# Performance work log

Hardware: AMD Instinct MI355X
Metric: run time of the kernel (lower is better)

## Reference

```python
import jax, jax.numpy as jnp
import numpy as np

B, T, C = 4, 1024, 1024
H, HKV, N = 16, 8, 64
REP = H // HKV
D_LORA, D_MV, D_GATE = 64, 32, 160
EPS = 1e-06
ROPE_THETA = 1000000.0


def setup_inputs() -> dict:
    key = jax.random.key(0)
    ks = jax.random.split(key, 20)
    def s(i, shape, sc=0.02, off=0.0):
        return jax.random.normal(ks[i], shape, jnp.float32) * sc + off
    return {
        "x": jax.random.normal(ks[0], (B, T, C), jnp.float32),
        "v_first": jax.random.normal(ks[1], (B, T, C), jnp.float32),
        "Wr": s(2, (C, H * N)), "Wk": s(3, (C, HKV * N)), "Wv": s(4, (C, HKV * N)), "Wo": s(5, (H * N, C)),
        "w0": s(6, (C,), 0.1, -4.0), "w1": s(7, (C, D_LORA)), "w2": s(8, (D_LORA, C)),
        "a0": s(9, (C,), 0.1), "a1": s(10, (C, D_LORA)), "a2": s(11, (D_LORA, C)),
        "v0": s(12, (C,), 0.1, 0.73), "v1": s(13, (C, D_MV)), "v2": s(14, (D_MV, C)),
        "g1": s(15, (C, D_GATE)), "g2": s(16, (D_GATE, C)),
        "r_k": s(17, (H, N), 0.1, -0.04),
        "r_norm_w": jnp.ones((N,), jnp.float32), "k_norm_w": jnp.ones((N,), jnp.float32),
    }


def rms_norm(x, w):
    var = jnp.mean(jnp.square(x.astype(jnp.float32)), axis=-1, keepdims=True)
    return w * (x.astype(jnp.float32) * jax.lax.rsqrt(var + EPS))


def rope_cos_sin(t, n):
    half = n // 2
    inv_freq = 1.0 / ROPE_THETA ** (jnp.arange(half, dtype=jnp.float32) / half)
    freqs = jnp.arange(t, dtype=jnp.float32)[:, None] * inv_freq[None, :]
    emb = jnp.concatenate([freqs, freqs], axis=-1)  # [T, N]
    # broadcast to [1, T, 1, N] (unsqueeze_dim=2 in the original)
    return jnp.cos(emb)[None, :, None, :], jnp.sin(emb)[None, :, None, :]


def rotate_half(x):
    x1, x2 = jnp.split(x, 2, axis=-1)
    return jnp.concatenate([-x2, x1], axis=-1)


def wkv7(r, dec, k, v, a, b):
    # RWKV-7 state recurrence. All inputs [B,T,H,N]; state S: [B,H,N_v,N_k].
    # S_t = S_{t-1} * diag(dec_t) + (S_{t-1} @ a_t) b_t^T + v_t k_t^T ; y_t = S_t r_t
    def step(S, ins):
        rt, wt, kt, vt, at, bt = ins  # each [B,H,N]
        S = S * wt[:, :, None, :] \
            + jnp.einsum('bhij,bhj,bhk->bhik', S, at, bt) \
            + vt[..., None] * kt[..., None, :]
        return S, jnp.einsum('bhij,bhj->bhi', S, rt)
    ins = tuple(jnp.moveaxis(t, 1, 0) for t in (r, dec, k, v, a, b))  # [T,B,H,N]
    S0 = jnp.zeros((r.shape[0], H, N, N), r.dtype)
    _, ys = jax.lax.scan(step, S0, ins)
    return jnp.moveaxis(ys, 0, 1)  # [B,T,H,N]


def _forward(x, v_first, Wr, Wk, Wv, Wo, w0, w1, w2, a0, a1, a2, v0, v1, v2, g1, g2, r_k, r_norm_w, k_norm_w):
    Bq, Tq = x.shape[0], x.shape[1]
    r = rms_norm((x @ Wr).reshape(Bq, Tq, H, N), r_norm_w)
    k = rms_norm((x @ Wk).reshape(Bq, Tq, HKV, N), k_norm_w)
    # w = -softplus(-(w0 + tanh(x@w1)@w2)) - 0.5 ; kernel decay = exp(-exp(w))
    w = -jax.nn.softplus(-(w0 + jnp.tanh(x @ w1) @ w2)) - 0.5  # [B,T,C]
    v = (x @ Wv).reshape(Bq, Tq, HKV, N)
    cos, sin = rope_cos_sin(Tq, N)
    r = r * cos + rotate_half(r) * sin
    k = k * cos + rotate_half(k) * sin
    k = jnp.repeat(k, REP, axis=2)  # GQA repeat -> [B,T,H,N]
    v = jnp.repeat(v, REP, axis=2)
    # layer_id != 0: residual value mixing with first-layer value
    mix = jax.nn.sigmoid(v0 + (x @ v1) @ v2).reshape(Bq, Tq, H, N)
    v = v + (v_first.reshape(Bq, Tq, H, N) - v) * mix
    a = jax.nn.sigmoid(a0 + (x @ a1) @ a2).reshape(Bq, Tq, H, N)
    g = jax.nn.sigmoid(x @ g1) @ g2  # [B,T,C]
    kk = k / jnp.maximum(jnp.linalg.norm(k, axis=-1, keepdims=True), 1e-12)  # F.normalize per head
    dec = jnp.exp(-jnp.exp(w)).reshape(Bq, Tq, H, N)
    y = wkv7(r, dec, k, v, -kk, kk * a)  # [B,T,H,N]
    y = y + jnp.sum(r * k * r_k, axis=-1, keepdims=True) * v
    out = (y.reshape(Bq, Tq, H * N) * g) @ Wo
    return out


def reference(x, v_first, Wr, Wk, Wv, Wo, w0, w1, w2, a0, a1, a2, v0, v1, v2, g1, g2, r_k, r_norm_w, k_norm_w):
    out = _forward(x, v_first, Wr, Wk, Wv, Wo, w0, w1, w2, a0, a1, a2, v0, v1, v2, g1, g2, r_k, r_norm_w, k_norm_w)
    return (out, v_first)
```

## Files before the change

### kernel.cpp

```cpp
#include <hip/hip_runtime.h>
#include <math.h>
#include <stdint.h>

#define Bb   4
#define Tt   1024
#define Cc   1024
#define Hh   16
#define HKVn 8
#define Nn   64
#define MT   (Bb*Tt)
#define NC   32
#define CL   32
#define NCAT 2432

typedef __bf16 bf16x8_t __attribute__((ext_vector_type(8)));
typedef float  f32x4_t  __attribute__((ext_vector_type(4)));

__device__ __forceinline__ uint16_t f2bf(float f) {
    uint32_t u = __float_as_uint(f);
    uint32_t r = (u + 0x7fffu + ((u >> 16) & 1u)) >> 16;
    return (uint16_t)r;
}

__device__ __forceinline__ float rlane(float v, int l) {
    return __uint_as_float(__builtin_amdgcn_readlane(__float_as_uint(v), l));
}

__device__ __forceinline__ void stage64(const float* g, float* l, int lane) {
    __builtin_amdgcn_global_load_lds(
        (const __attribute__((address_space(1))) uint32_t*)(g + lane),
        (__attribute__((address_space(3))) uint32_t*)l, 4, 0, 0);
}

__global__ __launch_bounds__(256) void conv_copy_kernel(
    const float* __restrict__ x, uint16_t* __restrict__ xb,
    const float4* __restrict__ vfi, float4* __restrict__ out2, int n4)
{
    int i = blockIdx.x * blockDim.x + threadIdx.x;
    if (i >= n4) return;
    float4 v = reinterpret_cast<const float4*>(x)[i];
    ushort4 o;
    o.x = f2bf(v.x); o.y = f2bf(v.y); o.z = f2bf(v.z); o.w = f2bf(v.w);
    reinterpret_cast<ushort4*>(xb)[i] = o;
    out2[i] = vfi[i];
}

__global__ __launch_bounds__(256) void transpose_all_kernel(
    const float* __restrict__ Wr, const float* __restrict__ Wk, const float* __restrict__ Wv,
    const float* __restrict__ w1, const float* __restrict__ a1, const float* __restrict__ v1,
    const float* __restrict__ g1, const float* __restrict__ Wo,
    const float* __restrict__ w2, const float* __restrict__ a2,
    const float* __restrict__ v2, const float* __restrict__ g2,
    uint16_t* __restrict__ WCAT, uint16_t* __restrict__ WoT,
    uint16_t* __restrict__ LW, uint16_t* __restrict__ LA,
    uint16_t* __restrict__ LV, uint16_t* __restrict__ LG)
{
    int z = blockIdx.z;
    const float* W; int Nsrc, Ndst, Ksrc, Kout, off; uint16_t* out;
    switch (z) {
        case 0:  W = Wr; Nsrc = 1024; Ndst = 1024; Ksrc = 1024; Kout = 1024; off = 0;    out = WCAT; break;
        case 1:  W = Wk; Nsrc = 512;  Ndst = 512;  Ksrc = 1024; Kout = 1024; off = 1024; out = WCAT; break;
        case 2:  W = Wv; Nsrc = 512;  Ndst = 512;  Ksrc = 1024; Kout = 1024; off = 1536; out = WCAT; break;
        case 3:  W = w1; Nsrc = 64;   Ndst = 64;   Ksrc = 1024; Kout = 1024; off = 2048; out = WCAT; break;
        case 4:  W = a1; Nsrc = 64;   Ndst = 64;   Ksrc = 1024; Kout = 1024; off = 2112; out = WCAT; break;
        case 5:  W = v1; Nsrc = 32;   Ndst = 64;   Ksrc = 1024; Kout = 1024; off = 2176; out = WCAT; break;
        case 6:  W = g1; Nsrc = 160;  Ndst = 192;  Ksrc = 1024; Kout = 1024; off = 2240; out = WCAT; break;
        case 7:  W = Wo; Nsrc = 1024; Ndst = 1024; Ksrc = 1024; Kout = 1024; off = 0;    out = WoT;  break;
        case 8:  W = w2; Nsrc = 1024; Ndst = 1024; Ksrc = 64;   Kout = 64;   off = 0;    out = LW;   break;
        case 9:  W = a2; Nsrc = 1024; Ndst = 1024; Ksrc = 64;   Kout = 64;   off = 0;    out = LA;   break;
        case 10: W = v2; Nsrc = 1024; Ndst = 1024; Ksrc = 32;   Kout = 64;   off = 0;    out = LV;   break;
        default: W = g2; Nsrc = 1024; Ndst = 1024; Ksrc = 160;  Kout = 192;  off = 0;    out = LG;   break;
    }
    int n0 = blockIdx.x * 32, k0 = blockIdx.y * 32;
    if (n0 >= Ndst || k0 >= Kout) return;
    __shared__ float tile[32][33];
    int tx = threadIdx.x & 31, ty = threadIdx.x >> 5;
    #pragma unroll
    for (int i = 0; i < 32; i += 8) {
        int k = k0 + ty + i, n = n0 + tx;
        tile[ty + i][tx] = (k < Ksrc && n < Nsrc) ? W[(size_t)k * Nsrc + n] : 0.f;
    }
    __syncthreads();
    #pragma unroll
    for (int i = 0; i < 32; i += 8) {
        int n = n0 + ty + i, k = k0 + tx;
        if (n < Ndst) out[(size_t)(off + n) * Kout + k] = f2bf(tile[tx][ty + i]);
    }
}

__global__ __launch_bounds__(256) void gemm_bf16_proj(
    const uint16_t* __restrict__ A, const uint16_t* __restrict__ Bt,
    int M, int N, int K,
    float* __restrict__ R_, float* __restrict__ K_, float* __restrict__ V_,
    uint16_t* __restrict__ W1b, uint16_t* __restrict__ A1b,
    uint16_t* __restrict__ V1b, uint16_t* __restrict__ G1b)
{
    __shared__ __align__(16) uint16_t As[128 * 64];
    __shared__ __align__(16) uint16_t Bs[128 * 64];
    int tid  = threadIdx.x;
    int lane = tid & 63, wid = tid >> 6;
    int wm = (wid >> 1) * 64, wn = (wid & 1) * 64;
    int bm = blockIdx.y * 128, bn = blockIdx.x * 128;

    f32x4_t acc[4][4];
    #pragma unroll
    for (int i = 0; i < 4; ++i)
        #pragma unroll
        for (int j = 0; j < 4; ++j)
            #pragma unroll
            for (int e = 0; e < 4; ++e) acc[i][j][e] = 0.f;

    int rowS[4], kbS[4];
    #pragma unroll
    for (int i = 0; i < 4; ++i) {
        int d = (i * 256 + tid) * 16;
        int row = d >> 7;
        int kb = (d & 127) ^ ((row & 7) << 4);
        rowS[i] = row; kbS[i] = kb >> 1;
    }

    for (int k0 = 0; k0 < K; k0 += 64) {
        #pragma unroll
        for (int i = 0; i < 4; ++i) {
            const uint16_t* srcA = A + (size_t)(bm + rowS[i]) * K + k0 + kbS[i];
            uint16_t* ldsA = As + (i * 256 + wid * 64) * 8;
            __builtin_amdgcn_global_load_lds(
                (const __attribute__((address_space(1))) uint32_t*)srcA,
                (__attribute__((address_space(3))) uint32_t*)ldsA, 16, 0, 0);
            int nr = bn + rowS[i];
            const uint16_t* srcB = Bt + (size_t)(nr < N ? nr : 0) * K + k0 + kbS[i];
            uint16_t* ldsB = Bs + (i * 256 + wid * 64) * 8;
            __builtin_amdgcn_global_load_lds(
                (const __attribute__((address_space(1))) uint32_t*)srcB,
                (__attribute__((address_space(3))) uint32_t*)ldsB, 16, 0, 0);
        }
        __syncthreads();

        #pragma unroll
        for (int kk = 0; kk < 64; kk += 32) {
            int fb = (kk + ((lane >> 4) << 3)) << 1;
            bf16x8_t af[4], bfr[4];
            #pragma unroll
            for (int i = 0; i < 4; ++i) {
                int row = wm + i * 16 + (lane & 15);
                int byteA = (row << 7) + (fb ^ ((row & 7) << 4));
                af[i] = *reinterpret_cast<const bf16x8_t*>(
                    reinterpret_cast<const char*>(As) + byteA);
                int col = wn + i * 16 + (lane & 15);
                int byteB = (col << 7) + (fb ^ ((col & 7) << 4));
                bfr[i] = *reinterpret_cast<const bf16x8_t*>(
                    reinterpret_cast<const char*>(Bs) + byteB);
            }
            #pragma unroll
            for (int i = 0; i < 4; ++i)
                #pragma unroll
                for (int j = 0; j < 4; ++j)
                    acc[i][j] = __builtin_amdgcn_mfma_f32_16x16x32_bf16(
                        af[i], bfr[j], acc[i][j], 0, 0, 0);
        }
        __syncthreads();
    }

    #pragma unroll
    for (int i = 0; i < 4; ++i) {
        int row0 = bm + wm + i * 16 + ((lane >> 4) << 2);
        #pragma unroll
        for (int j = 0; j < 4; ++j) {
            int col = bn + wn + j * 16 + (lane & 15);
            if (col >= N) continue;
            #pragma unroll
            for (int rg = 0; rg < 4; ++rg) {
                float v = acc[i][j][rg];
                int row = row0 + rg;
                if (col < 1024)       R_[(size_t)row * 1024 + col] = v;
                else if (col < 1536)  K_[(size_t)row * 512 + (col - 1024)] = v;
                else if (col < 2048)  V_[(size_t)row * 512 + (col - 1536)] = v;
                else if (col < 2112)  W1b[(size_t)row * 64 + (col - 2048)] = f2bf(tanhf(v));
                else if (col < 2176)  A1b[(size_t)row * 64 + (col - 2112)] = f2bf(v);
                else if (col < 2240)  V1b[(size_t)row * 64 + (col - 2176)] = f2bf(v);
                else                  G1b[(size_t)row * 192 + (col - 2240)] = f2bf(1.f / (1.f + expf(-v)));
            }
        }
    }
}

__global__ __launch_bounds__(256) void gemm_bf16(
    const uint16_t* __restrict__ A, const uint16_t* __restrict__ Bt,
    float* __restrict__ C, int M, int N, int K)
{
    __shared__ __align__(16) uint16_t As[128 * 64];
    __shared__ __align__(16) uint16_t Bs[128 * 64];
    int tid  = threadIdx.x;
    int lane = tid & 63, wid = tid >> 6;
    int wm = (wid >> 1) * 64, wn = (wid & 1) * 64;
    int bm = blockIdx.y * 128, bn = blockIdx.x * 128;

    f32x4_t acc[4][4];
    #pragma unroll
    for (int i = 0; i < 4; ++i)
        #pragma unroll
        for (int j = 0; j < 4; ++j)
            #pragma unroll
            for (int e = 0; e < 4; ++e) acc[i][j][e] = 0.f;

    int rowS[4], kbS[4];
    #pragma unroll
    for (int i = 0; i < 4; ++i) {
        int d = (i * 256 + tid) * 16;
        int row = d >> 7;
        int kb = (d & 127) ^ ((row & 7) << 4);
        rowS[i] = row; kbS[i] = kb >> 1;
    }

    for (int k0 = 0; k0 < K; k0 += 64) {
        #pragma unroll
        for (int i = 0; i < 4; ++i) {
            const uint16_t* srcA = A + (size_t)(bm + rowS[i]) * K + k0 + kbS[i];
            uint16_t* ldsA = As + (i * 256 + wid * 64) * 8;
            __builtin_amdgcn_global_load_lds(
                (const __attribute__((address_space(1))) uint32_t*)srcA,
                (__attribute__((address_space(3))) uint32_t*)ldsA, 16, 0, 0);
            int nr = bn + rowS[i];
            const uint16_t* srcB = Bt + (size_t)(nr < N ? nr : 0) * K + k0 + kbS[i];
            uint16_t* ldsB = Bs + (i * 256 + wid * 64) * 8;
            __builtin_amdgcn_global_load_lds(
                (const __attribute__((address_space(1))) uint32_t*)srcB,
                (__attribute__((address_space(3))) uint32_t*)ldsB, 16, 0, 0);
        }
        __syncthreads();

        #pragma unroll
        for (int kk = 0; kk < 64; kk += 32) {
            int fb = (kk + ((lane >> 4) << 3)) << 1;
            bf16x8_t af[4], bfr[4];
            #pragma unroll
            for (int i = 0; i < 4; ++i) {
                int row = wm + i * 16 + (lane & 15);
                int byteA = (row << 7) + (fb ^ ((row & 7) << 4));
                af[i] = *reinterpret_cast<const bf16x8_t*>(
                    reinterpret_cast<const char*>(As) + byteA);
                int col = wn + i * 16 + (lane & 15);
                int byteB = (col << 7) + (fb ^ ((col & 7) << 4));
                bfr[i] = *reinterpret_cast<const bf16x8_t*>(
                    reinterpret_cast<const char*>(Bs) + byteB);
            }
            #pragma unroll
            for (int i = 0; i < 4; ++i)
                #pragma unroll
                for (int j = 0; j < 4; ++j)
                    acc[i][j] = __builtin_amdgcn_mfma_f32_16x16x32_bf16(
                        af[i], bfr[j], acc[i][j], 0, 0, 0);
        }
        __syncthreads();
    }

    #pragma unroll
    for (int i = 0; i < 4; ++i) {
        int row0 = bm + wm + i * 16 + ((lane >> 4) << 2);
        #pragma unroll
        for (int j = 0; j < 4; ++j) {
            int col = bn + wn + j * 16 + (lane & 15);
            if (col >= N) continue;
            #pragma unroll
            for (int rg = 0; rg < 4; ++rg)
                C[(size_t)(row0 + rg) * N + col] = acc[i][j][rg];
        }
    }
}

__global__ __launch_bounds__(256) void lora2_mfma(
    const uint16_t* __restrict__ W1b, const uint16_t* __restrict__ A1b,
    const uint16_t* __restrict__ V1b, const uint16_t* __restrict__ G1b,
    const uint16_t* __restrict__ LW, const uint16_t* __restrict__ LA,
    const uint16_t* __restrict__ LV, const uint16_t* __restrict__ LG,
    const float* __restrict__ w0, const float* __restrict__ a0, const float* __restrict__ v0,
    const float* __restrict__ VRAW, const float* __restrict__ vfi,
    const float* __restrict__ ABUF,
    float* __restrict__ DEC, float* __restrict__ AARR,
    float* __restrict__ VFIN, float* __restrict__ GARR)
{
    int seg = blockIdx.x & 3;
    int bn = (blockIdx.x >> 2) * 128;
    int bm = blockIdx.y * 128;

    const uint16_t* A; const uint16_t* Bt; int K;
    if (seg == 0)      { A = W1b; Bt = LW; K = 64; }
    else if (seg == 1) { A = A1b; Bt = LA; K = 64; }
    else if (seg == 2) { A = V1b; Bt = LV; K = 64; }
    else               { A = G1b; Bt = LG; K = 192; }

    __shared__ __align__(16) uint16_t As[128 * 64];
    __shared__ __align__(16) uint16_t Bs[128 * 64];
    int tid  = threadIdx.x;
    int lane = tid & 63, wid = tid >> 6;
    int wm = (wid >> 1) * 64, wn = (wid & 1) * 64;

    f32x4_t acc[4][4];
    #pragma unroll
    for (int i = 0; i < 4; ++i)
        #pragma unroll
        for (int j = 0; j < 4; ++j)
            #pragma unroll
            for (int e = 0; e < 4; ++e) acc[i][j][e] = 0.f;

    int rowS[4], kbS[4];
    #pragma unroll
    for (int i = 0; i < 4; ++i) {
        int d = (i * 256 + tid) * 16;
        int row = d >> 7;
        int kb = (d & 127) ^ ((row & 7) << 4);
        rowS[i] = row; kbS[i] = kb >> 1;
    }

    for (int k0 = 0; k0 < K; k0 += 64) {
        #pragma unroll
        for (int i = 0; i < 4; ++i) {
            const uint16_t* srcA = A + (size_t)(bm + rowS[i]) * K + k0 + kbS[i];
            uint16_t* ldsA = As + (i * 256 + wid * 64) * 8;
            __builtin_amdgcn_global_load_lds(
                (const __attribute__((address_space(1))) uint32_t*)srcA,
                (__attribute__((address_space(3))) uint32_t*)ldsA, 16, 0, 0);
            const uint16_t* srcB = Bt + (size_t)(bn + rowS[i]) * K + k0 + kbS[i];
            uint16_t* ldsB = Bs + (i * 256 + wid * 64) * 8;
            __builtin_amdgcn_global_load_lds(
                (const __attribute__((address_space(1))) uint32_t*)srcB,
                (__attribute__((address_space(3))) uint32_t*)ldsB, 16, 0, 0);
        }
        __syncthreads();

        #pragma unroll
        for (int kk = 0; kk < 64; kk += 32) {
            int fb = (kk + ((lane >> 4) << 3)) << 1;
            bf16x8_t af[4], bfr[4];
            #pragma unroll
            for (int i = 0; i < 4; ++i) {
                int row = wm + i * 16 + (lane & 15);
                int byteA = (row << 7) + (fb ^ ((row & 7) << 4));
                af[i] = *reinterpret_cast<const bf16x8_t*>(
                    reinterpret_cast<const char*>(As) + byteA);
                int col = wn + i * 16 + (lane & 15);
                int byteB = (col << 7) + (fb ^ ((col & 7) << 4));
                bfr[i] = *reinterpret_cast<const bf16x8_t*>(
                    reinterpret_cast<const char*>(Bs) + byteB);
            }
            #pragma unroll
            for (int i = 0; i < 4; ++i)
                #pragma unroll
                for (int j = 0; j < 4; ++j)
                    acc[i][j] = __builtin_amdgcn_mfma_f32_16x16x32_bf16(
                        af[i], bfr[j], acc[i][j], 0, 0, 0);
        }
        __syncthreads();
    }

    #pragma unroll
    for (int i = 0; i < 4; ++i) {
        int row0 = bm + wm + i * 16 + ((lane >> 4) << 2);
        #pragma unroll
        for (int j = 0; j < 4; ++j) {
            int col = bn + wn + j * 16 + (lane & 15);
            #pragma unroll
            for (int rg = 0; rg < 4; ++rg) {
                float v = acc[i][j][rg];
                int row = row0 + rg;
                if (seg == 0) {
                    float z = v + w0[col];
                    float sig = 1.f / (1.f + expf(-z));
                    DEC[(size_t)row * 1024 + col] = expf(-0.6065306597f * sig);
                } else if (seg == 1) {
                    float kk = -ABUF[(size_t)row * 512 + ((col >> 7) << 6) + (col & 63)];
                    AARR[(size_t)row * 1024 + col] = kk / (1.f + expf(-(v + a0[col])));
                } else if (seg == 2) {
                    float m = 1.f / (1.f + expf(-(v + v0[col])));
                    float vr = VRAW[(size_t)row * 512 + ((col >> 7) << 6) + (col & 63)];
                    float vf = vfi[(size_t)row * 1024 + col];
                    VFIN[(size_t)row * 1024 + col] = vr + (vf - vr) * m;
                } else {
                    GARR[(size_t)row * 1024 + col] = v;
                }
            }
        }
    }
}

__global__ __launch_bounds__(64) void normrope_prep(
    float* __restrict__ RRAW, float* __restrict__ KRAW,
    float* __restrict__ ABUF,
    const float* __restrict__ rnw, const float* __restrict__ knw,
    const float* __restrict__ rk,
    float* __restrict__ BON)
{
    int blk = blockIdx.x;
    int hk = blk & 7;
    int bt = blk >> 3;
    int b = bt >> 10, t = bt & 1023;
    int lane = threadIdx.x;
    int fi = lane & 31;
    float invf = powf(1.0e6f, -(float)fi * (1.0f / 32.0f));
    float fr = (float)t * invf;
    float c = cosf(fr), s = sinf(fr);

    size_t kidx = ((size_t)bt * 8 + hk) * 64 + lane;
    float k = KRAW[kidx];
    float ss = k * k;
    #pragma unroll
    for (int m = 1; m < 64; m <<= 1) ss += __shfl_xor(ss, m, 64);
    float kn = k * rsqrtf(ss * (1.f / 64.f) + 1e-6f) * knw[lane];
    float kp = __shfl_xor(kn, 32, 64);
    float kroped = fmaf(kn, c, ((lane < 32) ? -kp : kp) * s);
    KRAW[kidx] = kroped;

    float ss2 = kroped * kroped;
    #pragma unroll
    for (int m = 1; m < 64; m <<= 1) ss2 += __shfl_xor(ss2, m, 64);
    float kk = kroped / fmaxf(sqrtf(ss2), 1e-12f);
    ABUF[kidx] = -kk;

    #pragma unroll
    for (int rep = 0; rep < 2; ++rep) {
        int h = hk * 2 + rep;
        size_t cidx = (size_t)bt * 1024 + h * 64 + lane;
        float r = RRAW[cidx];
        float ssr = r * r;
        #pragma unroll
        for (int m = 1; m < 64; m <<= 1) ssr += __shfl_xor(ssr, m, 64);
        float rn = r * rsqrtf(ssr * (1.f / 64.f) + 1e-6f) * rnw[lane];
        float rp = __shfl_xor(rn, 32, 64);
        float rroped = fmaf(rn, c, ((lane < 32) ? -rp : rp) * s);
        RRAW[cidx] = rroped;

        float bon = rroped * kroped * rk[h * 64 + lane];
        #pragma unroll
        for (int m = 1; m < 64; m <<= 1) bon += __shfl_xor(bon, m, 64);
        if (lane == 0) BON[((size_t)(b * 16 + h)) * 1024 + t] = bon;
    }
}

__global__ __launch_bounds__(64) void wkv_pass1(
    const float* __restrict__ R, const float* __restrict__ Kv,
    const float* __restrict__ Ab, const float* __restrict__ Bhat,
    const float* __restrict__ Dd, const float* __restrict__ Vv,
    float* __restrict__ Q, float* __restrict__ Y0,
    float* __restrict__ PLT, float* __restrict__ ZL)
{
    int blk = blockIdx.x;
    int c   = blk & (NC - 1);
    int bh  = blk >> 5;
    int h   = bh & 15;
    int b   = bh >> 4;
    int hk  = h >> 1;
    int lane = threadIdx.x;
    int t0 = c * CL;

    size_t cb = ((size_t)(b * 1024 + t0)) * 1024 + h * 64;
    size_t kb = ((size_t)(b * 1024 + t0)) * 512 + hk * 64;
    size_t qb = (((size_t)bh) * 1024 + t0) * 64;

    __shared__ __align__(16) float sA[2][64], sB[2][64], sD[2][64],
                                   sR[2][64], sK[2][64], sV[2][64];

    float SP[64], SZ[64];
    #pragma unroll
    for (int j = 0; j < 64; ++j) { SP[j] = (j == lane) ? 1.f : 0.f; SZ[j] = 0.f; }

    auto stage = [&](int u, int buf) {
        stage64(Ab   + kb + (size_t)u * 512,  &sA[buf][0], lane);
        stage64(Bhat + cb + (size_t)u * 1024, &sB[buf][0], lane);
        stage64(Dd   + cb + (size_t)u * 1024, &sD[buf][0], lane);
        stage64(R    + cb + (size_t)u * 1024, &sR[buf][0], lane);
        stage64(Kv   + kb + (size_t)u * 512,  &sK[buf][0], lane);
        stage64(Vv   + cb + (size_t)u * 1024, &sV[buf][0], lane);
    };
    stage(0, 0);

    for (int u = 0; u < CL; ++u) {
        int un = (u + 1 < CL) ? u + 1 : u;
        stage(un, (u + 1) & 1);
        asm volatile("s_waitcnt vmcnt(6)" ::: "memory");
        int cur = u & 1;
        float v = sV[cur][lane];

        float pa0 = 0.f, pa1 = 0.f, za0 = 0.f, za1 = 0.f;
        #pragma unroll
        for (int jc = 0; jc < 16; ++jc) {
            float4 a4 = *reinterpret_cast<const float4*>(&sA[cur][jc * 4]);
            pa0 = fmaf(SP[jc*4+0], a4.x, pa0); za0 = fmaf(SZ[jc*4+0], a4.x, za0);
            pa1 = fmaf(SP[jc*4+1], a4.y, pa1); za1 = fmaf(SZ[jc*4+1], a4.y, za1);
            pa0 = fmaf(SP[jc*4+2], a4.z, pa0); za0 = fmaf(SZ[jc*4+2], a4.z, za0);
            pa1 = fmaf(SP[jc*4+3], a4.w, pa1); za1 = fmaf(SZ[jc*4+3], a4.w, za1);
        }
        float pa = pa0 + pa1;
        float za = za0 + za1;

        float q0 = 0.f, q1 = 0.f, y0a = 0.f, y1a = 0.f;
        #pragma unroll
        for (int jc = 0; jc < 16; ++jc) {
            float4 d4 = *reinterpret_cast<const float4*>(&sD[cur][jc * 4]);
            float4 b4 = *reinterpret_cast<const float4*>(&sB[cur][jc * 4]);
            float4 k4 = *reinterpret_cast<const float4*>(&sK[cur][jc * 4]);
            float4 r4 = *reinterpret_cast<const float4*>(&sR[cur][jc * 4]);
            SP[jc*4+0] = fmaf(SP[jc*4+0], d4.x, pa * b4.x); q0  = fmaf(SP[jc*4+0], r4.x, q0);
            SZ[jc*4+0] = fmaf(SZ[jc*4+0], d4.x, fmaf(za, b4.x, v * k4.x)); y0a = fmaf(SZ[jc*4+0], r4.x, y0a);
            SP[jc*4+1] = fmaf(SP[jc*4+1], d4.y, pa * b4.y); q1  = fmaf(SP[jc*4+1], r4.y, q1);
            SZ[jc*4+1] = fmaf(SZ[jc*4+1], d4.y, fmaf(za, b4.y, v * k4.y)); y1a = fmaf(SZ[jc*4+1], r4.y, y1a);
            SP[jc*4+2] = fmaf(SP[jc*4+2], d4.z, pa * b4.z); q0  = fmaf(SP[jc*4+2], r4.z, q0);
            SZ[jc*4+2] = fmaf(SZ[jc*4+2], d4.z, fmaf(za, b4.z, v * k4.z)); y0a = fmaf(SZ[jc*4+2], r4.z, y0a);
            SP[jc*4+3] = fmaf(SP[jc*4+3], d4.w, pa * b4.w); q1  = fmaf(SP[jc*4+3], r4.w, q1);
            SZ[jc*4+3] = fmaf(SZ[jc*4+3], d4.w, fmaf(za, b4.w, v * k4.w)); y1a = fmaf(SZ[jc*4+3], r4.w, y1a);
        }
        Q[qb + (size_t)u * 64 + lane]    = q0 + q1;
        Y0[cb + (size_t)u * 1024 + lane] = y0a + y1a;
    }

    size_t pbT = (size_t)blk * 4096;
    #pragma unroll
    for (int j = 0; j < 64; ++j)
        PLT[pbT + j * 64 + (lane ^ ((j & 7) << 2))] = SP[j];
    size_t pb = pbT + (size_t)lane * 64;
    #pragma unroll
    for (int j = 0; j < 64; j += 4)
        *reinterpret_cast<float4*>(&ZL[pb + j]) =
            make_float4(SZ[j], SZ[j + 1], SZ[j + 2], SZ[j + 3]);
}

__global__ __launch_bounds__(256) void wkv_pass2(
    const float* __restrict__ PLT, float* ZLio)
{
    int blk = blockIdx.x;
    int rg  = blk & 3;
    int bh  = blk >> 2;
    int tid = threadIdx.x, lane = tid & 63, wv = tid >> 6;

    __shared__ __align__(16) float Pld[2][4096];
    __shared__ __align__(16) float Zld[2][1024];

    float S0 = 0.f, S1 = 0.f, S2 = 0.f, S3 = 0.f;

    auto stage = [&](int cc, int buf) {
        size_t pbase = ((size_t)bh * NC + cc) * 4096;
        #pragma unroll
        for (int i = 0; i < 4; ++i) {
            const float* src = PLT + pbase + (size_t)(i * 256 + tid) * 4;
            float* dst = &Pld[buf][(i * 256 + wv * 64) * 4];
            __builtin_amdgcn_global_load_lds(
                (const __attribute__((address_space(1))) uint32_t*)src,
                (__attribute__((address_space(3))) uint32_t*)dst, 16, 0, 0);
        }
        const float* zsrc = ZLio + pbase + (size_t)rg * 1024 + (size_t)tid * 4;
        float* zdst = &Zld[buf][wv * 256];
        __builtin_amdgcn_global_load_lds(
            (const __attribute__((address_space(1))) uint32_t*)zsrc,
            (__attribute__((address_space(3))) uint32_t*)zdst, 16, 0, 0);
    };

    stage(0, 0);

    for (int cc = 0; cc < NC; ++cc) {
        int cur = cc & 1;
        if (cc + 1 < NC) {
            stage(cc + 1, cur ^ 1);
            asm volatile("s_waitcnt vmcnt(5)" ::: "memory");
        } else {
            asm volatile("s_waitcnt vmcnt(0)" ::: "memory");
        }
        __syncthreads();

        size_t sb = ((size_t)bh * NC + cc) * 4096 + (size_t)(rg * 16 + wv * 4) * 64 + lane;
        ZLio[sb]       = S0;
        ZLio[sb + 64]  = S1;
        ZLio[sb + 128] = S2;
        ZLio[sb + 192] = S3;
        if (cc == NC - 1) break;

        int zb = (wv * 4) * 64 + lane;
        float acc0 = Zld[cur][zb],       acc1 = Zld[cur][zb + 64],
              acc2 = Zld[cur][zb + 128], acc3 = Zld[cur][zb + 192];
        const float* pcol = &Pld[cur][lane * 64];
        int swz = (lane & 7) << 2;
        #pragma unroll
        for (int m4 = 0; m4 < 64; m4 += 4) {
            float4 p4 = *reinterpret_cast<const float4*>(&pcol[m4 ^ swz]);
            #pragma unroll
            for (int s = 0; s < 4; ++s) {
                float pv = (&p4.x)[s];
                acc0 = fmaf(rlane(S0, m4 + s), pv, acc0);
                acc1 = fmaf(rlane(S1, m4 + s), pv, acc1);
                acc2 = fmaf(rlane(S2, m4 + s), pv, acc2);
                acc3 = fmaf(rlane(S3, m4 + s), pv, acc3);
            }
        }
        S0 = acc0; S1 = acc1; S2 = acc2; S3 = acc3;
        __syncthreads();
    }
}

__global__ __launch_bounds__(64) void wkv_pass3(
    const float* __restrict__ SST, const float* __restrict__ Q,
    const float* __restrict__ Vv, const float* __restrict__ G,
    const float* __restrict__ BON, const float* __restrict__ Y0,
    uint16_t* __restrict__ Yb)
{
    int blk = blockIdx.x;
    int c = blk & (NC - 1), bh = blk >> 5, h = bh & 15, b = bh >> 4;
    int lane = threadIdx.x;
    int t0 = c * CL;

    __shared__ __align__(16) float qs[2][64];
    __shared__ float bons[CL];
    if (lane < CL) bons[lane] = BON[((size_t)bh) * 1024 + t0 + lane];

    float S[64];
    size_t sb = ((size_t)blk) * 4096 + (size_t)lane * 64;
    #pragma unroll
    for (int jc = 0; jc < 16; ++jc) {
        float4 s4 = *reinterpret_cast<const float4*>(&SST[sb + jc * 4]);
        S[jc*4+0] = s4.x; S[jc*4+1] = s4.y; S[jc*4+2] = s4.z; S[jc*4+3] = s4.w;
    }

    size_t cb = ((size_t)(b * 1024 + t0)) * 1024 + h * 64 + lane;
    size_t qbase = (((size_t)bh) * 1024 + t0) * 64;

    stage64(Q + qbase, &qs[0][0], lane);
    for (int u = 0; u < CL; ++u) {
        int un = (u + 1 < CL) ? u + 1 : u;
        stage64(Q + qbase + (size_t)un * 64, &qs[(u + 1) & 1][0], lane);
        asm volatile("s_waitcnt vmcnt(1)" ::: "memory");
        int cur = u & 1;

        float d0 = 0.f, d1 = 0.f, d2 = 0.f, d3 = 0.f;
        #pragma unroll
        for (int jc = 0; jc < 16; ++jc) {
            float4 q4 = *reinterpret_cast<const float4*>(&qs[cur][jc * 4]);
            d0 = fmaf(S[jc*4+0], q4.x, d0);
            d1 = fmaf(S[jc*4+1], q4.y, d1);
            d2 = fmaf(S[jc*4+2], q4.z, d2);
            d3 = fmaf(S[jc*4+3], q4.w, d3);
        }
        float dot = (d0 + d1) + (d2 + d3);
        float y0 = Y0[cb + (size_t)u * 1024];
        float vc = Vv[cb + (size_t)u * 1024];
        float gc = G[cb + (size_t)u * 1024];
        float bon = bons[u];
        Yb[cb + (size_t)u * 1024] = f2bf((y0 + dot + bon * vc) * gc);
    }
}

extern "C" void kernel_launch(void* const* d_in, const int* in_sizes, int n_in,
                              void* d_out, int out_size, void* d_ws, size_t ws_size,
                              hipStream_t stream)
{
    const float* x   = (const float*)d_in[0];
    const float* vfi = (const float*)d_in[1];
    const float* Wr  = (const float*)d_in[2];
    const float* Wk  = (const float*)d_in[3];
    const float* Wv  = (const float*)d_in[4];
    const float* Wo  = (const float*)d_in[5];
    const float* w0  = (const float*)d_in[6];
    const float* w1  = (const float*)d_in[7];
    const float* w2  = (const float*)d_in[8];
    const float* a0  = (const float*)d_in[9];
    const float* a1  = (const float*)d_in[10];
    const float* a2  = (const float*)d_in[11];
    const float* v0  = (const float*)d_in[12];
    const float* v1  = (const float*)d_in[13];
    const float* v2  = (const float*)d_in[14];
    const float* g1  = (const float*)d_in[15];
    const float* g2  = (const float*)d_in[16];
    const float* rk  = (const float*)d_in[17];
    const float* rnw = (const float*)d_in[18];
    const float* knw = (const float*)d_in[19];

    float* ws = (float*)d_ws;
    size_t o = 0;
    float* RRAW = ws + o; o += (size_t)MT * 1024;
    float* KRAW = ws + o; o += (size_t)MT * 512;
    float* VRAW = ws + o; o += (size_t)MT * 512;
    float* DEC  = ws + o; o += (size_t)MT * 1024;
    float* AARR = ws + o; o += (size_t)MT * 1024;
    float* GARR = ws + o; o += (size_t)MT * 1024;
    float* VFIN = ws + o; o += (size_t)MT * 1024;
    float* YARR = ws + o; o += (size_t)MT * 1024;
    float* ABUF = ws + o; o += (size_t)MT * 512;
    float* QBUF = ws + o; o += (size_t)MT * 1024;
    float* PLB  = ws + o; o += (size_t)(Bb * Hh * NC) * 4096;
    float* ZLB  = ws + o; o += (size_t)(Bb * Hh * NC) * 4096;
    float* BON  = ws + o; o += (size_t)64 * 1024;
    uint16_t* XB   = (uint16_t*)(ws + o); o += (size_t)MT * 512;
    uint16_t* WCAT = (uint16_t*)(ws + o); o += (size_t)NCAT * 512;
    uint16_t* WoT  = (uint16_t*)(ws + o); o += (size_t)1024 * 512;
    uint16_t* W1b  = (uint16_t*)(ws + o); o += (size_t)MT * 32;
    uint16_t* A1b  = (uint16_t*)(ws + o); o += (size_t)MT * 32;
    uint16_t* V1b  = (uint16_t*)(ws + o); o += (size_t)MT * 32;
    uint16_t* G1b  = (uint16_t*)(ws + o); o += (size_t)MT * 96;
    uint16_t* LW   = (uint16_t*)(ws + o); o += (size_t)1024 * 32;
    uint16_t* LA   = (uint16_t*)(ws + o); o += (size_t)1024 * 32;
    uint16_t* LV   = (uint16_t*)(ws + o); o += (size_t)1024 * 32;
    uint16_t* LG   = (uint16_t*)(ws + o); o += (size_t)1024 * 96;
    uint16_t* YB = XB;

    conv_copy_kernel<<<dim3(MT * 1024 / 4 / 256), dim3(256), 0, stream>>>(
        x, XB, (const float4*)vfi, (float4*)((float*)d_out + (size_t)MT * 1024), MT * 1024 / 4);
    transpose_all_kernel<<<dim3(32, 32, 12), dim3(256), 0, stream>>>(
        Wr, Wk, Wv, w1, a1, v1, g1, Wo, w2, a2, v2, g2, WCAT, WoT, LW, LA, LV, LG);

    dim3 blk(256);

    gemm_bf16_proj<<<dim3(NCAT / 128, MT / 128), blk, 0, stream>>>(
        XB, WCAT, MT, NCAT, 1024, RRAW, KRAW, VRAW, W1b, A1b, V1b, G1b);

    normrope_prep<<<dim3(MT * HKVn), dim3(64), 0, stream>>>(
        RRAW, KRAW, ABUF, rnw, knw, rk, BON);

    lora2_mfma<<<dim3(32, MT / 128), blk, 0, stream>>>(
        W1b, A1b, V1b, G1b, LW, LA, LV, LG, w0, a0, v0, VRAW, vfi, ABUF,
        DEC, AARR, VFIN, GARR);

    wkv_pass1<<<dim3(Bb * Hh * NC), dim3(64), 0, stream>>>(
        RRAW, KRAW, ABUF, AARR, DEC, VFIN, QBUF, YARR, PLB, ZLB);
    wkv_pass2<<<dim3(Bb * Hh * 4), dim3(256), 0, stream>>>(PLB, ZLB);
    wkv_pass3<<<dim3(Bb * Hh * NC), dim3(64), 0, stream>>>(
        ZLB, QBUF, VFIN, GARR, BON, YARR, YB);

    gemm_bf16<<<dim3(1024 / 128, MT / 128), blk, 0, stream>>>(
        YB, WoT, (float*)d_out, MT, 1024, 1024);
}
```

Baseline: 402.7 us.

## Pack per-timestep WKV inputs into one interleaved record with bf16 a/b/k/r

Replaces the separate R, K, A, B, decay and V float arrays with one 1 KB packed record per (token, head). The record holds a, b, k and r as bf16 and decay and v as fp32, so the WKV recurrence stages each step with a single 16-byte global-to-LDS load per lane instead of six. The producer kernels (normrope_prep, lora2) now write directly into this layout, and the PLT buffer is aliased onto the no-longer-needed RRAW buffer. The aim is to cut memory traffic and load instructions in the latency-bound scan, at the cost of bf16 precision for r, k, a and b in the recurrence.

```diff
diff --git a/kernel.cpp b/kernel.cpp
--- a/kernel.cpp
+++ b/kernel.cpp
@@ -21,6 +21,8 @@
     uint32_t r = (u + 0x7fffu + ((u >> 16) & 1u)) >> 16;
     return (uint16_t)r;
 }
+#define BFLO(w) __uint_as_float((w) << 16)
+#define BFHI(w) __uint_as_float((w) & 0xffff0000u)
 
 __device__ __forceinline__ float rlane(float v, int l) {
     return __uint_as_float(__builtin_amdgcn_readlane(__float_as_uint(v), l));
@@ -31,6 +33,7 @@
         (const __attribute__((address_space(1))) uint32_t*)(g + lane),
         (__attribute__((address_space(3))) uint32_t*)l, 4, 0, 0);
 }
+
 
 __global__ __launch_bounds__(256) void conv_copy_kernel(
     const float* __restrict__ x, uint16_t* __restrict__ xb,
@@ -275,9 +278,7 @@
     const uint16_t* __restrict__ LV, const uint16_t* __restrict__ LG,
     const float* __restrict__ w0, const float* __restrict__ a0, const float* __restrict__ v0,
     const float* __restrict__ VRAW, const float* __restrict__ vfi,
-    const float* __restrict__ ABUF,
-    float* __restrict__ DEC, float* __restrict__ AARR,
-    float* __restrict__ VFIN, float* __restrict__ GARR)
+    char* __restrict__ PK, float* __restrict__ GARR)
 {
     int seg = blockIdx.x & 3;
     int bn = (blockIdx.x >> 2) * 128;
@@ -363,18 +364,22 @@
             for (int rg = 0; rg < 4; ++rg) {
                 float v = acc[i][j][rg];
                 int row = row0 + rg;
+                char* pkr = PK + (((size_t)row * 16) + (col >> 6)) * 1024;
+                int e = col & 63;
                 if (seg == 0) {
                     float z = v + w0[col];
                     float sig = 1.f / (1.f + expf(-z));
-                    DEC[(size_t)row * 1024 + col] = expf(-0.6065306597f * sig);
+                    *reinterpret_cast<float*>(pkr + 512 + 4 * e) = expf(-0.6065306597f * sig);
                 } else if (seg == 1) {
-                    float kk = -ABUF[(size_t)row * 512 + ((col >> 7) << 6) + (col & 63)];
-                    AARR[(size_t)row * 1024 + col] = kk / (1.f + expf(-(v + a0[col])));
+                    uint32_t araw = *reinterpret_cast<const uint16_t*>(pkr + 2 * e);
+                    float kk = -BFLO(araw);
+                    float bb = kk / (1.f + expf(-(v + a0[col])));
+                    *reinterpret_cast<uint16_t*>(pkr + 128 + 2 * e) = f2bf(bb);
                 } else if (seg == 2) {
                     float m = 1.f / (1.f + expf(-(v + v0[col])));
-                    float vr = VRAW[(size_t)row * 512 + ((col >> 7) << 6) + (col & 63)];
+                    float vr = VRAW[(size_t)row * 512 + ((col >> 7) << 6) + e];
                     float vf = vfi[(size_t)row * 1024 + col];
-                    VFIN[(size_t)row * 1024 + col] = vr + (vf - vr) * m;
+                    *reinterpret_cast<float*>(pkr + 768 + 4 * e) = vr + (vf - vr) * m;
                 } else {
                     GARR[(size_t)row * 1024 + col] = v;
                 }
@@ -384,8 +389,8 @@
 }
 
 __global__ __launch_bounds__(64) void normrope_prep(
-    float* __restrict__ RRAW, float* __restrict__ KRAW,
-    float* __restrict__ ABUF,
+    const float* __restrict__ RRAW, const float* __restrict__ KRAW,
+    char* __restrict__ PK,
     const float* __restrict__ rnw, const float* __restrict__ knw,
     const float* __restrict__ rk,
     float* __restrict__ BON)
@@ -408,13 +413,14 @@
     float kn = k * rsqrtf(ss * (1.f / 64.f) + 1e-6f) * knw[lane];
     float kp = __shfl_xor(kn, 32, 64);
     float kroped = fmaf(kn, c, ((lane < 32) ? -kp : kp) * s);
-    KRAW[kidx] = kroped;
 
     float ss2 = kroped * kroped;
     #pragma unroll
     for (int m = 1; m < 64; m <<= 1) ss2 += __shfl_xor(ss2, m, 64);
     float kk = kroped / fmaxf(sqrtf(ss2), 1e-12f);
-    ABUF[kidx] = -kk;
+
+    uint16_t a_bf = f2bf(-kk);
+    uint16_t k_bf = f2bf(kroped);
 
     #pragma unroll
     for (int rep = 0; rep < 2; ++rep) {
@@ -427,7 +433,11 @@
         float rn = r * rsqrtf(ssr * (1.f / 64.f) + 1e-6f) * rnw[lane];
         float rp = __shfl_xor(rn, 32, 64);
         float rroped = fmaf(rn, c, ((lane < 32) ? -rp : rp) * s);
-        RRAW[cidx] = rroped;
+
+        char* pkr = PK + (((size_t)bt * 16) + h) * 1024;
+        *reinterpret_cast<uint16_t*>(pkr + 2 * lane)       = a_bf;
+        *reinterpret_cast<uint16_t*>(pkr + 256 + 2 * lane) = k_bf;
+        *reinterpret_cast<uint16_t*>(pkr + 384 + 2 * lane) = f2bf(rroped);
 
         float bon = rroped * kroped * rk[h * 64 + lane];
         #pragma unroll
@@ -437,9 +447,7 @@
 }
 
 __global__ __launch_bounds__(64) void wkv_pass1(
-    const float* __restrict__ R, const float* __restrict__ Kv,
-    const float* __restrict__ Ab, const float* __restrict__ Bhat,
-    const float* __restrict__ Dd, const float* __restrict__ Vv,
+    const char* __restrict__ PK,
     float* __restrict__ Q, float* __restrict__ Y0,
     float* __restrict__ PLT, float* __restrict__ ZL)
 {
@@ -448,68 +456,110 @@
     int bh  = blk >> 5;
     int h   = bh & 15;
     int b   = bh >> 4;
-    int hk  = h >> 1;
     int lane = threadIdx.x;
     int t0 = c * CL;
-
-    size_t cb = ((size_t)(b * 1024 + t0)) * 1024 + h * 64;
-    size_t kb = ((size_t)(b * 1024 + t0)) * 512 + hk * 64;
+    int tb = b * 1024 + t0;
+
+    size_t cb = ((size_t)tb) * 1024 + h * 64;
     size_t qb = (((size_t)bh) * 1024 + t0) * 64;
 
-    __shared__ __align__(16) float sA[2][64], sB[2][64], sD[2][64],
-                                   sR[2][64], sK[2][64], sV[2][64];
+    __shared__ __align__(16) uint32_t pk[2][256];
 
     float SP[64], SZ[64];
     #pragma unroll
     for (int j = 0; j < 64; ++j) { SP[j] = (j == lane) ? 1.f : 0.f; SZ[j] = 0.f; }
 
     auto stage = [&](int u, int buf) {
-        stage64(Ab   + kb + (size_t)u * 512,  &sA[buf][0], lane);
-        stage64(Bhat + cb + (size_t)u * 1024, &sB[buf][0], lane);
-        stage64(Dd   + cb + (size_t)u * 1024, &sD[buf][0], lane);
-        stage64(R    + cb + (size_t)u * 1024, &sR[buf][0], lane);
-        stage64(Kv   + kb + (size_t)u * 512,  &sK[buf][0], lane);
-        stage64(Vv   + cb + (size_t)u * 1024, &sV[buf][0], lane);
+        const char* src = PK + (((size_t)(tb + u)) * 16 + h) * 1024 + lane * 16;
+        __builtin_amdgcn_global_load_lds(
+            (const __attribute__((address_space(1))) uint32_t*)src,
+            (__attribute__((address_space(3))) uint32_t*)&pk[buf][0], 16, 0, 0);
     };
     stage(0, 0);
 
     for (int u = 0; u < CL; ++u) {
         int un = (u + 1 < CL) ? u + 1 : u;
         stage(un, (u + 1) & 1);
-        asm volatile("s_waitcnt vmcnt(6)" ::: "memory");
+        asm volatile("s_waitcnt vmcnt(1)" ::: "memory");
         int cur = u & 1;
-        float v = sV[cur][lane];
+        const uint32_t* aw = &pk[cur][0];
+        const uint32_t* bw = &pk[cur][32];
+        const uint32_t* kw = &pk[cur][64];
+        const uint32_t* rw = &pk[cur][96];
+        const float*    dp = reinterpret_cast<const float*>(&pk[cur][128]);
+        float v = reinterpret_cast<const float*>(&pk[cur][192])[lane];
 
         float pa0 = 0.f, pa1 = 0.f, za0 = 0.f, za1 = 0.f;
         #pragma unroll
-        for (int jc = 0; jc < 16; ++jc) {
-            float4 a4 = *reinterpret_cast<const float4*>(&sA[cur][jc * 4]);
-            pa0 = fmaf(SP[jc*4+0], a4.x, pa0); za0 = fmaf(SZ[jc*4+0], a4.x, za0);
-            pa1 = fmaf(SP[jc*4+1], a4.y, pa1); za1 = fmaf(SZ[jc*4+1], a4.y, za1);
-            pa0 = fmaf(SP[jc*4+2], a4.z, pa0); za0 = fmaf(SZ[jc*4+2], a4.z, za0);
-            pa1 = fmaf(SP[jc*4+3], a4.w, pa1); za1 = fmaf(SZ[jc*4+3], a4.w, za1);
+        for (int jc = 0; jc < 8; ++jc) {
+            uint4 a4 = *reinterpret_cast<const uint4*>(aw + jc * 4);
+            int j = jc * 8;
+            float f0 = BFLO(a4.x), f1 = BFHI(a4.x), f2 = BFLO(a4.y), f3 = BFHI(a4.y);
+            float f4 = BFLO(a4.z), f5 = BFHI(a4.z), f6 = BFLO(a4.w), f7 = BFHI(a4.w);
+            pa0 = fmaf(SP[j+0], f0, pa0); za0 = fmaf(SZ[j+0], f0, za0);
+            pa1 = fmaf(SP[j+1], f1, pa1); za1 = fmaf(SZ[j+1], f1, za1);
+            pa0 = fmaf(SP[j+2], f2, pa0); za0 = fmaf(SZ[j+2], f2, za0);
+            pa1 = fmaf(SP[j+3], f3, pa1); za1 = fmaf(SZ[j+3], f3, za1);
+            pa0 = fmaf(SP[j+4], f4, pa0); za0 = fmaf(SZ[j+4], f4, za0);
+            pa1 = fmaf(SP[j+5], f5, pa1); za1 = fmaf(SZ[j+5], f5, za1);
+            pa0 = fmaf(SP[j+6], f6, pa0); za0 = fmaf(SZ[j+6], f6, za0);
+            pa1 = fmaf(SP[j+7], f7, pa1); za1 = fmaf(SZ[j+7], f7, za1);
         }
         float pa = pa0 + pa1;
         float za = za0 + za1;
 
-        float q0 = 0.f, q1 = 0.f, y0a = 0.f, y1a = 0.f;
-        #pragma unroll
-        for (int jc = 0; jc < 16; ++jc) {
-            float4 d4 = *reinterpret_cast<const float4*>(&sD[cur][jc * 4]);
-            float4 b4 = *reinterpret_cast<const float4*>(&sB[cur][jc * 4]);
-            float4 k4 = *reinterpret_cast<const float4*>(&sK[cur][jc * 4]);
-            float4 r4 = *reinterpret_cast<const float4*>(&sR[cur][jc * 4]);
-            SP[jc*4+0] = fmaf(SP[jc*4+0], d4.x, pa * b4.x); q0  = fmaf(SP[jc*4+0], r4.x, q0);
-            SZ[jc*4+0] = fmaf(SZ[jc*4+0], d4.x, fmaf(za, b4.x, v * k4.x)); y0a = fmaf(SZ[jc*4+0], r4.x, y0a);
-            SP[jc*4+1] = fmaf(SP[jc*4+1], d4.y, pa * b4.y); q1  = fmaf(SP[jc*4+1], r4.y, q1);
-            SZ[jc*4+1] = fmaf(SZ[jc*4+1], d4.y, fmaf(za, b4.y, v * k4.y)); y1a = fmaf(SZ[jc*4+1], r4.y, y1a);
-            SP[jc*4+2] = fmaf(SP[jc*4+2], d4.z, pa * b4.z); q0  = fmaf(SP[jc*4+2], r4.z, q0);
-            SZ[jc*4+2] = fmaf(SZ[jc*4+2], d4.z, fmaf(za, b4.z, v * k4.z)); y0a = fmaf(SZ[jc*4+2], r4.z, y0a);
-            SP[jc*4+3] = fmaf(SP[jc*4+3], d4.w, pa * b4.w); q1  = fmaf(SP[jc*4+3], r4.w, q1);
-            SZ[jc*4+3] = fmaf(SZ[jc*4+3], d4.w, fmaf(za, b4.w, v * k4.w)); y1a = fmaf(SZ[jc*4+3], r4.w, y1a);
+        float q0 = 0.f, q1 = 0.f, ya0 = 0.f, ya1 = 0.f;
+        #pragma unroll
+        for (int jc = 0; jc < 8; ++jc) {
+            uint4 b4 = *reinterpret_cast<const uint4*>(bw + jc * 4);
+            uint4 k4 = *reinterpret_cast<const uint4*>(kw + jc * 4);
+            uint4 r4 = *reinterpret_cast<const uint4*>(rw + jc * 4);
+            float4 dA = *reinterpret_cast<const float4*>(dp + jc * 8);
+            float4 dB = *reinterpret_cast<const float4*>(dp + jc * 8 + 4);
+            int j = jc * 8;
+            {
+                float bf = BFLO(b4.x), kf = BFLO(k4.x), rf = BFLO(r4.x), df = dA.x;
+                SP[j+0] = fmaf(SP[j+0], df, pa * bf); q0  = fmaf(SP[j+0], rf, q0);
+                SZ[j+0] = fmaf(SZ[j+0], df, fmaf(za, bf, v * kf)); ya0 = fmaf(SZ[j+0], rf, ya0);
+            }
+            {
+                float bf = BFHI(b4.x), kf = BFHI(k4.x), rf = BFHI(r4.x), df = dA.y;
+                SP[j+1] = fmaf(SP[j+1], df, pa * bf); q1  = fmaf(SP[j+1], rf, q1);
+                SZ[j+1] = fmaf(SZ[j+1], df, fmaf(za, bf, v * kf)); ya1 = fmaf(SZ[j+1], rf, ya1);
+            }
+            {
+                float bf = BFLO(b4.y), kf = BFLO(k4.y), rf = BFLO(r4.y), df = dA.z;
+                SP[j+2] = fmaf(SP[j+2], df, pa * bf); q0  = fmaf(SP[j+2], rf, q0);
+                SZ[j+2] = fmaf(SZ[j+2], df, fmaf(za, bf, v * kf)); ya0 = fmaf(SZ[j+2], rf, ya0);
+            }
+            {
+                float bf = BFHI(b4.y), kf = BFHI(k4.y), rf = BFHI(r4.y), df = dA.w;
+                SP[j+3] = fmaf(SP[j+3], df, pa * bf); q1  = fmaf(SP[j+3], rf, q1);
+                SZ[j+3] = fmaf(SZ[j+3], df, fmaf(za, bf, v * kf)); ya1 = fmaf(SZ[j+3], rf, ya1);
+            }
+            {
+                float bf = BFLO(b4.z), kf = BFLO(k4.z), rf = BFLO(r4.z), df = dB.x;
+                SP[j+4] = fmaf(SP[j+4], df, pa * bf); q0  = fmaf(SP[j+4], rf, q0);
+                SZ[j+4] = fmaf(SZ[j+4], df, fmaf(za, bf, v * kf)); ya0 = fmaf(SZ[j+4], rf, ya0);
+            }
+            {
+                float bf = BFHI(b4.z), kf = BFHI(k4.z), rf = BFHI(r4.z), df = dB.y;
+                SP[j+5] = fmaf(SP[j+5], df, pa * bf); q1  = fmaf(SP[j+5], rf, q1);
+                SZ[j+5] = fmaf(SZ[j+5], df, fmaf(za, bf, v * kf)); ya1 = fmaf(SZ[j+5], rf, ya1);
+            }
+            {
+                float bf = BFLO(b4.w), kf = BFLO(k4.w), rf = BFLO(r4.w), df = dB.z;
+                SP[j+6] = fmaf(SP[j+6], df, pa * bf); q0  = fmaf(SP[j+6], rf, q0);
+                SZ[j+6] = fmaf(SZ[j+6], df, fmaf(za, bf, v * kf)); ya0 = fmaf(SZ[j+6], rf, ya0);
+            }
+            {
+                float bf = BFHI(b4.w), kf = BFHI(k4.w), rf = BFHI(r4.w), df = dB.w;
+                SP[j+7] = fmaf(SP[j+7], df, pa * bf); q1  = fmaf(SP[j+7], rf, q1);
+                SZ[j+7] = fmaf(SZ[j+7], df, fmaf(za, bf, v * kf)); ya1 = fmaf(SZ[j+7], rf, ya1);
+            }
         }
         Q[qb + (size_t)u * 64 + lane]    = q0 + q1;
-        Y0[cb + (size_t)u * 1024 + lane] = y0a + y1a;
+        Y0[cb + (size_t)u * 1024 + lane] = ya0 + ya1;
     }
 
     size_t pbT = (size_t)blk * 4096;
@@ -596,7 +646,7 @@
 
 __global__ __launch_bounds__(64) void wkv_pass3(
     const float* __restrict__ SST, const float* __restrict__ Q,
-    const float* __restrict__ Vv, const float* __restrict__ G,
+    const char* __restrict__ PK, const float* __restrict__ G,
     const float* __restrict__ BON, const float* __restrict__ Y0,
     uint16_t* __restrict__ Yb)
 {
@@ -604,6 +654,7 @@
     int c = blk & (NC - 1), bh = blk >> 5, h = bh & 15, b = bh >> 4;
     int lane = threadIdx.x;
     int t0 = c * CL;
+    int tb = b * 1024 + t0;
 
     __shared__ __align__(16) float qs[2][64];
     __shared__ float bons[CL];
@@ -617,7 +668,7 @@
         S[jc*4+0] = s4.x; S[jc*4+1] = s4.y; S[jc*4+2] = s4.z; S[jc*4+3] = s4.w;
     }
 
-    size_t cb = ((size_t)(b * 1024 + t0)) * 1024 + h * 64 + lane;
+    size_t cb = ((size_t)tb) * 1024 + h * 64 + lane;
     size_t qbase = (((size_t)bh) * 1024 + t0) * 64;
 
     stage64(Q + qbase, &qs[0][0], lane);
@@ -638,7 +689,8 @@
         }
         float dot = (d0 + d1) + (d2 + d3);
         float y0 = Y0[cb + (size_t)u * 1024];
-        float vc = Vv[cb + (size_t)u * 1024];
+        float vc = *(reinterpret_cast<const float*>(
+            PK + (((size_t)(tb + u)) * 16 + h) * 1024 + 768) + lane);
         float gc = G[cb + (size_t)u * 1024];
         float bon = bons[u];
         Yb[cb + (size_t)u * 1024] = f2bf((y0 + dot + bon * vc) * gc);
@@ -675,16 +727,13 @@
     float* RRAW = ws + o; o += (size_t)MT * 1024;
     float* KRAW = ws + o; o += (size_t)MT * 512;
     float* VRAW = ws + o; o += (size_t)MT * 512;
-    float* DEC  = ws + o; o += (size_t)MT * 1024;
-    float* AARR = ws + o; o += (size_t)MT * 1024;
+    float* PLT  = RRAW;
+    float* ZLB  = ws + o; o += (size_t)(Bb * Hh * NC) * 4096;
     float* GARR = ws + o; o += (size_t)MT * 1024;
-    float* VFIN = ws + o; o += (size_t)MT * 1024;
     float* YARR = ws + o; o += (size_t)MT * 1024;
-    float* ABUF = ws + o; o += (size_t)MT * 512;
     float* QBUF = ws + o; o += (size_t)MT * 1024;
-    float* PLB  = ws + o; o += (size_t)(Bb * Hh * NC) * 4096;
-    float* ZLB  = ws + o; o += (size_t)(Bb * Hh * NC) * 4096;
     float* BON  = ws + o; o += (size_t)64 * 1024;
+    char*  PK   = (char*)(ws + o); o += (size_t)MT * 4096;
     uint16_t* XB   = (uint16_t*)(ws + o); o += (size_t)MT * 512;
     uint16_t* WCAT = (uint16_t*)(ws + o); o += (size_t)NCAT * 512;
     uint16_t* WoT  = (uint16_t*)(ws + o); o += (size_t)1024 * 512;
@@ -709,17 +758,16 @@
         XB, WCAT, MT, NCAT, 1024, RRAW, KRAW, VRAW, W1b, A1b, V1b, G1b);
 
     normrope_prep<<<dim3(MT * HKVn), dim3(64), 0, stream>>>(
-        RRAW, KRAW, ABUF, rnw, knw, rk, BON);
+        RRAW, KRAW, PK, rnw, knw, rk, BON);
 
     lora2_mfma<<<dim3(32, MT / 128), blk, 0, stream>>>(
-        W1b, A1b, V1b, G1b, LW, LA, LV, LG, w0, a0, v0, VRAW, vfi, ABUF,
-        DEC, AARR, VFIN, GARR);
+        W1b, A1b, V1b, G1b, LW, LA, LV, LG, w0, a0, v0, VRAW, vfi, PK, GARR);
 
     wkv_pass1<<<dim3(Bb * Hh * NC), dim3(64), 0, stream>>>(
-        RRAW, KRAW, ABUF, AARR, DEC, VFIN, QBUF, YARR, PLB, ZLB);
-    wkv_pass2<<<dim3(Bb * Hh * 4), dim3(256), 0, stream>>>(PLB, ZLB);
+        PK, QBUF, YARR, PLT, ZLB);
+    wkv_pass2<<<dim3(Bb * Hh * 4), dim3(256), 0, stream>>>(PLT, ZLB);
     wkv_pass3<<<dim3(Bb * Hh * NC), dim3(64), 0, stream>>>(
-        ZLB, QBUF, VFIN, GARR, BON, YARR, YB);
+        ZLB, QBUF, PK, GARR, BON, YARR, YB);
 
     gemm_bf16<<<dim3(1024 / 128, MT / 128), blk, 0, stream>>>(
         YB, WoT, (float*)d_out, MT, 1024, 1024);
```

Result: slower. 466.1 us (+15.7%).
